# Performance work log

Hardware: AMD Instinct MI355X
Metric: run time of the kernel (lower is better)

The kernel has to match this reference:

```python
import jax, jax.numpy as jnp
import numpy as np

N_NODES = 50000


def setup_inputs() -> dict:
    key = jax.random.key(0)
    k1, k2, k3, k4 = jax.random.split(key, 4)
    N, E, D_IN, D_OUT = N_NODES, 1_600_000, 128, 128
    x = jax.random.normal(k1, (N, D_IN), dtype=jnp.float32)
    edge_index = jax.random.randint(k2, (2, E), 0, N, dtype=jnp.int64)
    W = jax.random.normal(k3, (D_IN, D_OUT), dtype=jnp.float32) * (1.0 / np.sqrt(D_IN))
    b = jax.random.normal(k4, (D_OUT,), dtype=jnp.float32) * 0.01
    return {"x": x, "edge_index": edge_index, "W": W, "b": b}


def reference(x, edge_index, W, b):
    N = x.shape[0]
    # add self loops: edge (i, i) for every node
    loops = jnp.arange(N, dtype=edge_index.dtype)
    row = jnp.concatenate([edge_index[0], loops])  # [E+N]
    col = jnp.concatenate([edge_index[1], loops])  # [E+N]
    # degree over col (matches torch_geometric degree(col, N))
    deg = jax.ops.segment_sum(jnp.ones_like(col, dtype=x.dtype), col, num_segments=N)
    deg_inv_sqrt = jnp.where(deg > 0, jax.lax.rsqrt(jnp.maximum(deg, 1.0)), 0.0)
    norm = deg_inv_sqrt[row] * deg_inv_sqrt[col]  # [E+N]
    # linear transform then gather-multiply-scatter (segment sum over row)
    xl = x @ W + b  # [N, D_OUT]
    msg = norm[:, None] * xl[col]  # [E+N, D_OUT]
    out = jax.ops.segment_sum(msg, row, num_segments=N)
    return out
```

## Files before the change

### kernel.cpp

```cpp
#include <hip/hip_runtime.h>
#include <hip/hip_bf16.h>


#define D     128
#define TILE  8192
#define BINB  1024
#define RPB   256
#define MAXB  256
#define SPLIT_CAP 16384
#define DSEG  2
#define DTIL  32

typedef short  bf16x8 __attribute__((ext_vector_type(8)));
typedef float  f32x4  __attribute__((ext_vector_type(4)));
typedef unsigned short us4 __attribute__((ext_vector_type(4)));
typedef unsigned short us8 __attribute__((ext_vector_type(8)));

static __device__ __forceinline__ unsigned short f2bf(float f) {
    unsigned u = __float_as_uint(f);
    u = (u + 0x7FFFu + ((u >> 16) & 1u)) >> 16;
    return (unsigned short)u;
}
static __device__ __forceinline__ float bf2f(unsigned short s) {
    return __uint_as_float(((unsigned)s) << 16);
}

__global__ __launch_bounds__(256) void k_prep(const float* __restrict__ W,
                                              unsigned short* __restrict__ wtb,
                                              int* __restrict__ cntc,
                                              int* __restrict__ bcur,
                                              int N, int NB, int CAP) {
    int i = blockIdx.x * 256 + threadIdx.x;
    if (i < N) cntc[i] = 0;
    if (i < NB) bcur[i] = i * CAP;
    if (i < D * D) {
        int n = i >> 7, k = i & 127;
        wtb[n * 128 + k] = f2bf(W[k * 128 + n]);
    }
}

__global__ __launch_bounds__(BINB) void k_bin(const int* __restrict__ rows,
                                              const int* __restrict__ cols,
                                              int* __restrict__ bcur,
                                              unsigned* __restrict__ ebuf,
                                              int E, int NB, int CAP) {
    __shared__ int lcnt[MAXB];
    __shared__ int lbase[MAXB];
    const int t = threadIdx.x;
    const int base = blockIdx.x * TILE;
    int m = E - base; if (m > TILE) m = TILE;

    unsigned p[TILE / BINB];
    #pragma unroll
    for (int it = 0; it < TILE / BINB; ++it) {
        int i = it * BINB + t;
        if (i < m) {
            unsigned r = (unsigned)rows[base + i];
            unsigned c = (unsigned)cols[base + i];
            p[it] = c | ((r & 255u) << 16) | ((r >> 8) << 24);
        }
    }
    for (int b = t; b < NB; b += BINB) lcnt[b] = 0;
    __syncthreads();
    #pragma unroll
    for (int it = 0; it < TILE / BINB; ++it) {
        int i = it * BINB + t;
        if (i < m) atomicAdd(&lcnt[p[it] >> 24], 1);
    }
    __syncthreads();
    for (int b = t; b < NB; b += BINB) {
        int c = lcnt[b];
        lbase[b] = c ? atomicAdd(&bcur[b], c) : 0;
        lcnt[b] = 0;
    }
    __syncthreads();
    #pragma unroll
    for (int it = 0; it < TILE / BINB; ++it) {
        int i = it * BINB + t;
        if (i < m) {
            int bk = p[it] >> 24;
            int r  = atomicAdd(&lcnt[bk], 1);
            int pos = lbase[bk] + r;
            if (pos < (bk + 1) * CAP)
                ebuf[pos] = p[it] & 0xFFFFFFu;
        }
    }
}

__global__ __launch_bounds__(1024) void k_deg2(const int* __restrict__ cols,
                                               int* __restrict__ cntc,
                                               int E, int N) {
    const int segw = (N + DSEG - 1) / DSEG;
    __shared__ int h[25088];
    const int seg  = blockIdx.x & (DSEG - 1);
    const int tile = blockIdx.x >> 1;
    const int lo = seg * segw;
    const int hi = min(lo + segw, N);
    const int w  = hi - lo;
    for (int i = threadIdx.x; i < w; i += 1024) h[i] = 0;
    __syncthreads();
    const int per = (E + DTIL - 1) / DTIL;
    const int beg = tile * per;
    const int end = min(beg + per, E);
    for (int i = beg + threadIdx.x; i < end; i += 1024) {
        int c = cols[i];
        if (c >= lo && c < hi) atomicAdd(&h[c - lo], 1);
    }
    __syncthreads();
    for (int i = threadIdx.x; i < w; i += 1024) {
        int v = h[i];
        if (v) atomicAdd(&cntc[lo + i], v);
    }
}

__global__ __launch_bounds__(256) void k_dis(const int* __restrict__ cntc,
                                             float* __restrict__ dis, int N) {
    int i = blockIdx.x * 256 + threadIdx.x;
    if (i < N) dis[i] = rsqrtf((float)(cntc[i] + 1));
}

__global__ __launch_bounds__(1024) void k_split(const int* __restrict__ bcur,
                                                const unsigned* __restrict__ ebuf,
                                                unsigned short* __restrict__ ecol,
                                                int* __restrict__ begN,
                                                int* __restrict__ endN,
                                                int N, int CAP) {
    __shared__ unsigned short sorted[SPLIT_CAP];
    __shared__ int cnt[RPB];
    __shared__ int excl[RPB];
    __shared__ int cur[RPB];
    const int b = blockIdx.x, t = threadIdx.x;
    const int base = b * CAP;
    int m = bcur[b] - base; if (m > CAP) m = CAP;
    if (t < RPB) cnt[t] = 0;
    __syncthreads();
    for (int i = t; i < m; i += 1024)
        atomicAdd(&cnt[(ebuf[base + i] >> 16) & 255], 1);
    __syncthreads();
    if (t == 0) {
        int s = 0;
        #pragma unroll
        for (int r = 0; r < RPB; ++r) { excl[r] = s; s += cnt[r]; }
    }
    __syncthreads();
    const int row0 = b * RPB;
    if (t < RPB) {
        cur[t] = excl[t];
        if (row0 + t < N) {
            begN[row0 + t] = base + excl[t];
            endN[row0 + t] = base + excl[t] + cnt[t];
        }
    }
    __syncthreads();
    for (int i = t; i < m; i += 1024) {
        unsigned p = ebuf[base + i];
        int pos = atomicAdd(&cur[(p >> 16) & 255], 1);
        sorted[pos] = (unsigned short)(p & 0xFFFFu);
    }
    __syncthreads();
    for (int i = t; i < m; i += 1024)
        ecol[base + i] = sorted[i];
}

__global__ __launch_bounds__(256) void k_gemm(const float* __restrict__ x,
                                              const unsigned short* __restrict__ wtb,
                                              const float* __restrict__ bia,
                                              unsigned short* __restrict__ xlb,
                                              int N) {
    __shared__ unsigned short wt[128][136];
    __shared__ unsigned short xs[64][136];
    const int t = threadIdx.x;
    const int row0 = blockIdx.x * 64;

    #pragma unroll
    for (int i = 0; i < 8; ++i) {
        int j = i * 256 + t;
        int n = j >> 4, k8 = j & 15;
        us8 v = *(const us8*)&wtb[j * 8];
        *(us8*)&wt[n][k8 * 8] = v;
    }
    #pragma unroll
    for (int i = 0; i < 8; ++i) {
        int j = i * 256 + t;
        int r = j >> 5, c4 = j & 31;
        int gr = row0 + r;
        us4 o = (us4){0, 0, 0, 0};
        if (gr < N) {
            float4 v = *(const float4*)&x[(size_t)gr * D + c4 * 4];
            o = (us4){f2bf(v.x), f2bf(v.y), f2bf(v.z), f2bf(v.w)};
        }
        *(us4*)&xs[r][c4 * 4] = o;
    }
    __syncthreads();

    const int w  = t >> 6, l = t & 63;
    const int m0 = w * 16;
    const int lm = l & 15, lq = l >> 4;

    f32x4 acc[8];
    #pragma unroll
    for (int nt = 0; nt < 8; ++nt) acc[nt] = (f32x4){0.f, 0.f, 0.f, 0.f};

    #pragma unroll
    for (int kk = 0; kk < 4; ++kk) {
        const int kof = kk * 32 + lq * 8;
        bf16x8 a = *(const bf16x8*)&xs[m0 + lm][kof];
        #pragma unroll
        for (int nt = 0; nt < 8; ++nt) {
            bf16x8 bb = *(const bf16x8*)&wt[nt * 16 + lm][kof];
            acc[nt] = __builtin_amdgcn_mfma_f32_16x16x32_bf16(a, bb, acc[nt], 0, 0, 0);
        }
    }

    #pragma unroll
    for (int nt = 0; nt < 8; ++nt) {
        const int col = nt * 16 + lm;
        const float bc = bia[col];
        #pragma unroll
        for (int r = 0; r < 4; ++r) {
            int grow = row0 + m0 + lq * 4 + r;
            if (grow < N) xlb[(size_t)grow * D + col] = f2bf(acc[nt][r] + bc);
        }
    }
}

__global__ __launch_bounds__(256) void k_reduce(const int* __restrict__ begN,
                                                const int* __restrict__ endN,
                                                const unsigned short* __restrict__ ecol,
                                                const float* __restrict__ dis,
                                                const unsigned short* __restrict__ xlb,
                                                float* __restrict__ out, int N) {
    const int wave = threadIdx.x >> 6;
    const int lane = threadIdx.x & 63;
    const int i = blockIdx.x * 4 + wave;
    if (i >= N) return;
    const float di = dis[i];

    const ushort2 sv = *reinterpret_cast<const ushort2*>(xlb + (size_t)i * D + lane * 2);
    float ax = di * di * bf2f(sv.x);
    float ay = di * di * bf2f(sv.y);

    const int beg = begN[i], end = endN[i];
    for (int base = beg; base < end; base += 64) {
        int m = end - base; if (m > 64) m = 64;
        int   c = 0;
        float n = 0.0f;
        if (lane < m) {
            c = ecol[base + lane];
            n = di * dis[c];
        }
        for (int j = 0; j < m; j += 8) {
            float vx[8], vy[8], nn[8];
            #pragma unroll
            for (int u = 0; u < 8; ++u) {
                int cc = __shfl(c, j + u);
                ushort2 s = *reinterpret_cast<const ushort2*>(xlb + (size_t)cc * D + lane * 2);
                vx[u] = bf2f(s.x);
                vy[u] = bf2f(s.y);
                nn[u] = __shfl(n, j + u);
            }
            #pragma unroll
            for (int u = 0; u < 8; ++u) {
                ax = fmaf(nn[u], vx[u], ax);
                ay = fmaf(nn[u], vy[u], ay);
            }
        }
    }
    *reinterpret_cast<float2*>(out + (size_t)i * D + lane * 2) = make_float2(ax, ay);
}

__global__ __launch_bounds__(256) void k_zero(int* __restrict__ p, int n) {
    int i = blockIdx.x * 256 + threadIdx.x;
    if (i < n) p[i] = 0;
}
__global__ __launch_bounds__(256) void k_deg(const int* __restrict__ cols,
                                             int* __restrict__ cntc, int E) {
    int e = blockIdx.x * 256 + threadIdx.x;
    if (e < E) atomicAdd(&cntc[cols[e]], 1);
}
#define GEMM_R 8
__global__ __launch_bounds__(128) void k_gemmf(const float* __restrict__ x,
                                               const float* __restrict__ W,
                                               const float* __restrict__ b,
                                               float* __restrict__ xl, int N) {
    __shared__ float xs[GEMM_R][D];
    const int c  = threadIdx.x;
    const int r0 = blockIdx.x * GEMM_R;
    #pragma unroll
    for (int r = 0; r < GEMM_R; ++r) {
        int row = r0 + r;
        xs[r][c] = (row < N) ? x[row * D + c] : 0.0f;
    }
    __syncthreads();
    float acc[GEMM_R];
    const float bc = b[c];
    #pragma unroll
    for (int r = 0; r < GEMM_R; ++r) acc[r] = bc;
    for (int k = 0; k < D; k += 4) {
        const float w0 = W[(k + 0) * D + c];
        const float w1 = W[(k + 1) * D + c];
        const float w2 = W[(k + 2) * D + c];
        const float w3 = W[(k + 3) * D + c];
        #pragma unroll
        for (int r = 0; r < GEMM_R; ++r) {
            const float4 xv = *reinterpret_cast<const float4*>(&xs[r][k]);
            acc[r] = fmaf(xv.x, w0, acc[r]);
            acc[r] = fmaf(xv.y, w1, acc[r]);
            acc[r] = fmaf(xv.z, w2, acc[r]);
            acc[r] = fmaf(xv.w, w3, acc[r]);
        }
    }
    #pragma unroll
    for (int r = 0; r < GEMM_R; ++r) {
        int row = r0 + r;
        if (row < N) xl[row * D + c] = acc[r];
    }
}
__global__ __launch_bounds__(256) void k_self(const float* __restrict__ xl,
                                              const float* __restrict__ dis,
                                              float* __restrict__ out, int N) {
    int gid = blockIdx.x * 256 + threadIdx.x;
    int i = gid >> 7;
    if (i < N) {
        float d = dis[i];
        out[gid] = d * d * xl[gid];
    }
}
__global__ __launch_bounds__(256) void k_scatter(const int* __restrict__ rows,
                                                 const int* __restrict__ cols,
                                                 const float* __restrict__ dis,
                                                 const float* __restrict__ xl,
                                                 float* __restrict__ out, int E) {
    long long gid = (long long)blockIdx.x * 256 + threadIdx.x;
    int e    = (int)(gid >> 6);
    int lane = (int)(gid & 63);
    if (e >= E) return;
    const int row = rows[e];
    const int col = cols[e];
    const float nrm = dis[row] * dis[col];
    atomicAdd(&out[row * D + lane],      nrm * xl[col * D + lane]);
    atomicAdd(&out[row * D + 64 + lane], nrm * xl[col * D + 64 + lane]);
}

extern "C" void kernel_launch(void* const* d_in, const int* in_sizes, int n_in,
                              void* d_out, int out_size, void* d_ws, size_t ws_size,
                              hipStream_t stream) {
    const float* x   = (const float*)d_in[0];
    const int*   ei  = (const int*)d_in[1];
    const float* W   = (const float*)d_in[2];
    const float* b   = (const float*)d_in[3];
    float*       out = (float*)d_out;

    const int N = in_sizes[0] / D;
    const int E = in_sizes[1] / 2;
    const int* rows = ei;
    const int* cols = ei + E;
    const int NB = (N + RPB - 1) / RPB;
    const int NT = (E + TILE - 1) / TILE;
    const int CAP = (((2 * E) / NB) + 63) / 64 * 64;

    char* p = (char*)d_ws;
    size_t off = 0;
    unsigned short* xlb  = (unsigned short*)(p + off); off += (size_t)N * D * 2;
    unsigned short* wtb  = (unsigned short*)(p + off); off += (size_t)D * D * 2;
    float*          dis  = (float*)(p + off);          off += (size_t)N * 4;
    int*            cntc = (int*)(p + off);            off += (size_t)N * 4;
    int*            bcur = (int*)(p + off);            off += (size_t)MAXB * 4;
    int*            begN = (int*)(p + off);            off += (size_t)N * 4;
    int*            endN = (int*)(p + off);            off += (size_t)N * 4;
    unsigned*       ebuf = (unsigned*)(p + off);       off += (size_t)NB * CAP * 4;
    unsigned short* ecol = (unsigned short*)(p + off); off += (size_t)NB * CAP * 2;

    const int gN = (N + 255) / 256;
    const int gE = (E + 255) / 256;

    if (N <= 65536 && NB <= MAXB && CAP <= SPLIT_CAP && ws_size >= off) {
        k_prep  <<<gN, 256, 0, stream>>>(W, wtb, cntc, bcur, N, NB, CAP);
        k_bin   <<<NT, BINB, 0, stream>>>(rows, cols, bcur, ebuf, E, NB, CAP);
        k_deg2  <<<DTIL * DSEG, 1024, 0, stream>>>(cols, cntc, E, N);
        k_dis   <<<gN, 256, 0, stream>>>(cntc, dis, N);
        k_split <<<NB, 1024, 0, stream>>>(bcur, ebuf, ecol, begN, endN, N, CAP);
        k_gemm  <<<(N + 63) / 64, 256, 0, stream>>>(x, wtb, b, xlb, N);
        k_reduce<<<(N + 3) / 4, 256, 0, stream>>>(begN, endN, ecol, dis, xlb, out, N);
    } else {
        char* q = (char*)d_ws;
        float* xl   = (float*)q;
        float* disF = (float*)(q + (size_t)N * D * 4);
        int*   cc   = (int*)(q + (size_t)N * D * 4 + (size_t)N * 4);
        k_zero <<<gN, 256, 0, stream>>>(cc, N);
        k_deg  <<<gE, 256, 0, stream>>>(cols, cc, E);
        k_dis  <<<gN, 256, 0, stream>>>(cc, disF, N);
        k_gemmf<<<(N + GEMM_R - 1) / GEMM_R, 128, 0, stream>>>(x, W, b, xl, N);
        k_self <<<((N * D) + 255) / 256, 256, 0, stream>>>(xl, disF, out, N);
        long long st = (long long)E * 64;
        k_scatter<<<(int)((st + 255) / 256), 256, 0, stream>>>(rows, cols, disF, xl, out, E);
    }
}
```

Before: 199.0 us.

## Fuse degree counting into binning pass and locally sort tiles before global scatter

The separate column-degree histogram pass (k_deg2) and the k_dis kernel are removed. k_bin now also bins edges by column bucket into a byte buffer, and a new k_degdis kernel counts per-node degree from that buffer and writes the rsqrt normalisation. k_bin also sorts each tile locally in shared memory before writing, so global writes are grouped by bucket, and it halves the tile size. The serial prefix sum in k_split is replaced with a wavefront shuffle scan. In exchange the binning kernel uses more shared memory and atomics, and a second edge buffer is written and read.

```diff
diff --git a/kernel.cpp b/kernel.cpp
--- a/kernel.cpp
+++ b/kernel.cpp
@@ -3,13 +3,11 @@
 
 
 #define D     128
-#define TILE  8192
+#define TILE  4096
 #define BINB  1024
 #define RPB   256
 #define MAXB  256
 #define SPLIT_CAP 16384
-#define DSEG  2
-#define DTIL  32
 
 typedef short  bf16x8 __attribute__((ext_vector_type(8)));
 typedef float  f32x4  __attribute__((ext_vector_type(4)));
@@ -27,12 +25,11 @@
 
 __global__ __launch_bounds__(256) void k_prep(const float* __restrict__ W,
                                               unsigned short* __restrict__ wtb,
-                                              int* __restrict__ cntc,
                                               int* __restrict__ bcur,
-                                              int N, int NB, int CAP) {
+                                              int* __restrict__ bcurC,
+                                              int NB, int CAP, int CAPC) {
     int i = blockIdx.x * 256 + threadIdx.x;
-    if (i < N) cntc[i] = 0;
-    if (i < NB) bcur[i] = i * CAP;
+    if (i < NB) { bcur[i] = i * CAP; bcurC[i] = i * CAPC; }
     if (i < D * D) {
         int n = i >> 7, k = i & 127;
         wtb[n * 128 + k] = f2bf(W[k * 128 + n]);
@@ -42,15 +39,20 @@
 __global__ __launch_bounds__(BINB) void k_bin(const int* __restrict__ rows,
                                               const int* __restrict__ cols,
                                               int* __restrict__ bcur,
+                                              int* __restrict__ bcurC,
                                               unsigned* __restrict__ ebuf,
-                                              int E, int NB, int CAP) {
-    __shared__ int lcnt[MAXB];
-    __shared__ int lbase[MAXB];
+                                              unsigned char* __restrict__ cebuf,
+                                              int E, int NB, int CAP, int CAPC) {
+    __shared__ unsigned sorted[TILE];
+    __shared__ unsigned short sortedC[TILE];
+    __shared__ int lcnt[MAXB], lbase[MAXB], excl[MAXB], cur[MAXB];
+    __shared__ int lcntC[MAXB], lbaseC[MAXB], exclC[MAXB], curC[MAXB];
     const int t = threadIdx.x;
     const int base = blockIdx.x * TILE;
     int m = E - base; if (m > TILE) m = TILE;
 
     unsigned p[TILE / BINB];
+    unsigned short q[TILE / BINB];
     #pragma unroll
     for (int it = 0; it < TILE / BINB; ++it) {
         int i = it * BINB + t;
@@ -58,65 +60,96 @@
             unsigned r = (unsigned)rows[base + i];
             unsigned c = (unsigned)cols[base + i];
             p[it] = c | ((r & 255u) << 16) | ((r >> 8) << 24);
-        }
-    }
-    for (int b = t; b < NB; b += BINB) lcnt[b] = 0;
+            q[it] = (unsigned short)c;
+        }
+    }
+    for (int b = t; b < MAXB; b += BINB) { lcnt[b] = 0; lcntC[b] = 0; }
     __syncthreads();
     #pragma unroll
     for (int it = 0; it < TILE / BINB; ++it) {
         int i = it * BINB + t;
-        if (i < m) atomicAdd(&lcnt[p[it] >> 24], 1);
-    }
-    __syncthreads();
+        if (i < m) {
+            atomicAdd(&lcnt[p[it] >> 24], 1);
+            atomicAdd(&lcntC[q[it] >> 8], 1);
+        }
+    }
+    __syncthreads();
+    if (t < 64) {
+        int b4 = t * 4;
+        int v0 = lcnt[b4], v1 = lcnt[b4+1], v2 = lcnt[b4+2], v3 = lcnt[b4+3];
+        int s = v0+v1+v2+v3, inc = s;
+        #pragma unroll
+        for (int off = 1; off < 64; off <<= 1) { int o = __shfl_up(inc, off); if (t >= off) inc += o; }
+        int ex = inc - s;
+        excl[b4] = ex; excl[b4+1] = ex+v0; excl[b4+2] = ex+v0+v1; excl[b4+3] = ex+v0+v1+v2;
+    } else if (t < 128) {
+        int l = t - 64, b4 = l * 4;
+        int v0 = lcntC[b4], v1 = lcntC[b4+1], v2 = lcntC[b4+2], v3 = lcntC[b4+3];
+        int s = v0+v1+v2+v3, inc = s;
+        #pragma unroll
+        for (int off = 1; off < 64; off <<= 1) { int o = __shfl_up(inc, off); if (l >= off) inc += o; }
+        int ex = inc - s;
+        exclC[b4] = ex; exclC[b4+1] = ex+v0; exclC[b4+2] = ex+v0+v1; exclC[b4+3] = ex+v0+v1+v2;
+    }
     for (int b = t; b < NB; b += BINB) {
         int c = lcnt[b];
         lbase[b] = c ? atomicAdd(&bcur[b], c) : 0;
-        lcnt[b] = 0;
-    }
+        int cc = lcntC[b];
+        lbaseC[b] = cc ? atomicAdd(&bcurC[b], cc) : 0;
+    }
+    __syncthreads();
+    for (int b = t; b < NB; b += BINB) { cur[b] = excl[b]; curC[b] = exclC[b]; }
     __syncthreads();
     #pragma unroll
     for (int it = 0; it < TILE / BINB; ++it) {
         int i = it * BINB + t;
         if (i < m) {
-            int bk = p[it] >> 24;
-            int r  = atomicAdd(&lcnt[bk], 1);
-            int pos = lbase[bk] + r;
-            if (pos < (bk + 1) * CAP)
-                ebuf[pos] = p[it] & 0xFFFFFFu;
-        }
-    }
-}
-
-__global__ __launch_bounds__(1024) void k_deg2(const int* __restrict__ cols,
-                                               int* __restrict__ cntc,
-                                               int E, int N) {
-    const int segw = (N + DSEG - 1) / DSEG;
-    __shared__ int h[25088];
-    const int seg  = blockIdx.x & (DSEG - 1);
-    const int tile = blockIdx.x >> 1;
-    const int lo = seg * segw;
-    const int hi = min(lo + segw, N);
-    const int w  = hi - lo;
-    for (int i = threadIdx.x; i < w; i += 1024) h[i] = 0;
-    __syncthreads();
-    const int per = (E + DTIL - 1) / DTIL;
-    const int beg = tile * per;
-    const int end = min(beg + per, E);
-    for (int i = beg + threadIdx.x; i < end; i += 1024) {
-        int c = cols[i];
-        if (c >= lo && c < hi) atomicAdd(&h[c - lo], 1);
-    }
-    __syncthreads();
-    for (int i = threadIdx.x; i < w; i += 1024) {
-        int v = h[i];
-        if (v) atomicAdd(&cntc[lo + i], v);
-    }
-}
-
-__global__ __launch_bounds__(256) void k_dis(const int* __restrict__ cntc,
-                                             float* __restrict__ dis, int N) {
-    int i = blockIdx.x * 256 + threadIdx.x;
-    if (i < N) dis[i] = rsqrtf((float)(cntc[i] + 1));
+            int pos  = atomicAdd(&cur[p[it] >> 24], 1);
+            sorted[pos] = p[it];
+            int posC = atomicAdd(&curC[q[it] >> 8], 1);
+            sortedC[posC] = q[it];
+        }
+    }
+    __syncthreads();
+    #pragma unroll
+    for (int it = 0; it < TILE / BINB; ++it) {
+        int i = it * BINB + t;
+        if (i < m) {
+            unsigned pp = sorted[i];
+            int bk = pp >> 24;
+            int g  = lbase[bk] + i - excl[bk];
+            if (g < (bk + 1) * CAP) ebuf[g] = pp & 0xFFFFFFu;
+            unsigned short qq = sortedC[i];
+            int bc = qq >> 8;
+            int gc = lbaseC[bc] + i - exclC[bc];
+            if (gc < (bc + 1) * CAPC) cebuf[gc] = (unsigned char)(qq & 255u);
+        }
+    }
+}
+
+__global__ __launch_bounds__(256) void k_degdis(const int* __restrict__ bcurC,
+                                                const unsigned char* __restrict__ cebuf,
+                                                float* __restrict__ dis,
+                                                int N, int CAPC) {
+    __shared__ int cnt[RPB];
+    const int b = blockIdx.x, t = threadIdx.x;
+    const int base = b * CAPC;
+    int m = bcurC[b] - base; if (m > CAPC) m = CAPC;
+    cnt[t] = 0;
+    __syncthreads();
+    const unsigned* cw = (const unsigned*)(cebuf + base);
+    int nw = m >> 2;
+    for (int i = t; i < nw; i += 256) {
+        unsigned u = cw[i];
+        atomicAdd(&cnt[u & 255u], 1);
+        atomicAdd(&cnt[(u >> 8) & 255u], 1);
+        atomicAdd(&cnt[(u >> 16) & 255u], 1);
+        atomicAdd(&cnt[u >> 24], 1);
+    }
+    if (t < (m & 3)) atomicAdd(&cnt[cebuf[base + nw * 4 + t]], 1);
+    __syncthreads();
+    int node = b * RPB + t;
+    if (node < N) dis[node] = rsqrtf((float)(cnt[t] + 1));
 }
 
 __global__ __launch_bounds__(1024) void k_split(const int* __restrict__ bcur,
@@ -137,10 +170,14 @@
     for (int i = t; i < m; i += 1024)
         atomicAdd(&cnt[(ebuf[base + i] >> 16) & 255], 1);
     __syncthreads();
-    if (t == 0) {
-        int s = 0;
-        #pragma unroll
-        for (int r = 0; r < RPB; ++r) { excl[r] = s; s += cnt[r]; }
+    if (t < 64) {
+        int b4 = t * 4;
+        int v0 = cnt[b4], v1 = cnt[b4+1], v2 = cnt[b4+2], v3 = cnt[b4+3];
+        int s = v0+v1+v2+v3, inc = s;
+        #pragma unroll
+        for (int off = 1; off < 64; off <<= 1) { int o = __shfl_up(inc, off); if (t >= off) inc += o; }
+        int ex = inc - s;
+        excl[b4] = ex; excl[b4+1] = ex+v0; excl[b4+2] = ex+v0+v1; excl[b4+3] = ex+v0+v1+v2;
     }
     __syncthreads();
     const int row0 = b * RPB;
@@ -278,6 +315,11 @@
     int e = blockIdx.x * 256 + threadIdx.x;
     if (e < E) atomicAdd(&cntc[cols[e]], 1);
 }
+__global__ __launch_bounds__(256) void k_dis(const int* __restrict__ cntc,
+                                             float* __restrict__ dis, int N) {
+    int i = blockIdx.x * 256 + threadIdx.x;
+    if (i < N) dis[i] = rsqrtf((float)(cntc[i] + 1));
+}
 #define GEMM_R 8
 __global__ __launch_bounds__(128) void k_gemmf(const float* __restrict__ x,
                                                const float* __restrict__ W,
@@ -357,28 +399,29 @@
     const int* cols = ei + E;
     const int NB = (N + RPB - 1) / RPB;
     const int NT = (E + TILE - 1) / TILE;
-    const int CAP = (((2 * E) / NB) + 63) / 64 * 64;
+    const int CAP  = (((2 * E) / NB) + 63) / 64 * 64;
+    const int CAPC = CAP;
 
     char* p = (char*)d_ws;
     size_t off = 0;
-    unsigned short* xlb  = (unsigned short*)(p + off); off += (size_t)N * D * 2;
-    unsigned short* wtb  = (unsigned short*)(p + off); off += (size_t)D * D * 2;
-    float*          dis  = (float*)(p + off);          off += (size_t)N * 4;
-    int*            cntc = (int*)(p + off);            off += (size_t)N * 4;
-    int*            bcur = (int*)(p + off);            off += (size_t)MAXB * 4;
-    int*            begN = (int*)(p + off);            off += (size_t)N * 4;
-    int*            endN = (int*)(p + off);            off += (size_t)N * 4;
-    unsigned*       ebuf = (unsigned*)(p + off);       off += (size_t)NB * CAP * 4;
-    unsigned short* ecol = (unsigned short*)(p + off); off += (size_t)NB * CAP * 2;
+    unsigned short* xlb   = (unsigned short*)(p + off); off += (size_t)N * D * 2;
+    unsigned short* wtb   = (unsigned short*)(p + off); off += (size_t)D * D * 2;
+    float*          dis   = (float*)(p + off);          off += (size_t)N * 4;
+    int*            bcur  = (int*)(p + off);            off += (size_t)MAXB * 4;
+    int*            bcurC = (int*)(p + off);            off += (size_t)MAXB * 4;
+    int*            begN  = (int*)(p + off);            off += (size_t)N * 4;
+    int*            endN  = (int*)(p + off);            off += (size_t)N * 4;
+    unsigned*       ebuf  = (unsigned*)(p + off);       off += (size_t)NB * CAP * 4;
+    unsigned short* ecol  = (unsigned short*)(p + off); off += (size_t)NB * CAP * 2;
+    unsigned char*  cebuf = (unsigned char*)(p + off);  off += (size_t)NB * CAPC;
 
     const int gN = (N + 255) / 256;
     const int gE = (E + 255) / 256;
 
     if (N <= 65536 && NB <= MAXB && CAP <= SPLIT_CAP && ws_size >= off) {
-        k_prep  <<<gN, 256, 0, stream>>>(W, wtb, cntc, bcur, N, NB, CAP);
-        k_bin   <<<NT, BINB, 0, stream>>>(rows, cols, bcur, ebuf, E, NB, CAP);
-        k_deg2  <<<DTIL * DSEG, 1024, 0, stream>>>(cols, cntc, E, N);
-        k_dis   <<<gN, 256, 0, stream>>>(cntc, dis, N);
+        k_prep  <<<(D * D + 255) / 256, 256, 0, stream>>>(W, wtb, bcur, bcurC, NB, CAP, CAPC);
+        k_bin   <<<NT, BINB, 0, stream>>>(rows, cols, bcur, bcurC, ebuf, cebuf, E, NB, CAP, CAPC);
+        k_degdis<<<NB, 256, 0, stream>>>(bcurC, cebuf, dis, N, CAPC);
         k_split <<<NB, 1024, 0, stream>>>(bcur, ebuf, ecol, begN, endN, N, CAP);
         k_gemm  <<<(N + 63) / 64, 256, 0, stream>>>(x, wtb, b, xlb, N);
         k_reduce<<<(N + 3) / 4, 256, 0, stream>>>(begN, endN, ecol, dis, xlb, out, N);
```

New measurement: 177.5 us. 1.12x faster.
